# Kernel optimization log

Hardware: AMD Instinct MI355X
Metric: run time of the kernel (lower is better)

The kernel has to match this reference:

```python
import jax, jax.numpy as jnp
import numpy as np

N = 307      # fixed number of graph nodes
C_IN = 5     # input channels
H = 16       # hidden width
K = 6        # Chebyshev orders (K_init=5 -> K+1=6)
LSTM_H = 32  # NL LSTM hidden
B = 512      # batch


def setup_inputs() -> dict:
    key = jax.random.key(0)
    ks = jax.random.split(key, 16)
    s = lambda i, shape, sc=0.1: jax.random.normal(ks[i], shape, jnp.float32) * sc
    return dict(
        flow_x=jax.random.normal(ks[0], (B, N, C_IN), jnp.float32),
        node_emb=jax.random.uniform(ks[1], (N, 10), jnp.float32),  # torch.rand init
        cheb_w=s(2, (K, C_IN, H)),
        cheb_b=jnp.zeros((H,), jnp.float32),
        cou_w=s(3, (C_IN, H)),
        gl_out=s(4, (H, H)),
        gl_fk=s(5, (H, H)),
        gl_tz_w=s(6, (H, H)),
        gl_tz_b=jnp.zeros((H,), jnp.float32),
        lstm_Wih=s(7, (H, 4 * LSTM_H)),
        lstm_b=jnp.zeros((4 * LSTM_H,), jnp.float32),  # b_ih + b_hh combined
        nl_w2=s(8, (LSTM_H, H)),
        c_w=s(9, (H, H)),
        c_b=jnp.zeros((H,), jnp.float32),
        c1_w=s(10, (H, H)),
        c1_b=jnp.zeros((H,), jnp.float32),
    )


def reference(flow_x, node_emb, cheb_w, cheb_b, cou_w, gl_out, gl_fk, gl_tz_w,
              gl_tz_b, lstm_Wih, lstm_b, nl_w2, c_w, c_b, c1_w, c1_b):
    # graph = cosine_similarity(node_embeddings.detach()) -> no grad to node_emb
    E = jax.lax.stop_gradient(node_emb)
    En = E / jnp.linalg.norm(E, axis=1, keepdims=True)
    G = En @ En.T                                            # [N,N]
    # normalized Laplacian L = I - D^-1/2 G D^-1/2
    d = jnp.sum(G, axis=-1) ** -0.5
    I = jnp.eye(N, dtype=G.dtype)
    L = I - (d[:, None] * G) * d[None, :]

    # Chebyshev polynomial stack T_0..T_{K-1}
    Ts = [I, L]
    for _ in range(K - 2):
        Ts.append(2.0 * (L @ Ts[-1]) - Ts[-2])
    polys = jnp.stack(Ts)                                    # [K,N,N]

    out = flow_x @ cou_w                                     # [B,N,H]
    hk = jnp.einsum('knm,bmc->kbnc', polys, flow_x)          # [K,B,N,C]
    output = jnp.einsum('kbnc,kcd->bnd', hk, cheb_w) + cheb_b  # [B,N,H]

    def GL(data):
        o1 = jnp.einsum('nm,bmc->bnc', L, data)
        o3 = jnp.tanh(jnp.tanh(data @ gl_out) @ gl_fk)
        return (o1 - o3) @ gl_tz_w + gl_tz_b

    def NL(data):
        # single-step LSTM cell with zero initial state, then tanh, then linear
        g = data @ lstm_Wih + lstm_b
        i, f, gg, o = jnp.split(g, 4, axis=-1)  # torch gate order i,f,g,o
        c = jax.nn.sigmoid(i) * jnp.tanh(gg)    # c0=0 -> forget term vanishes
        hh = jax.nn.sigmoid(o) * jnp.tanh(c)
        return jnp.tanh(hh) @ nl_w2

    # RK4-like GL diffusion chain: res_1..res_8, step_0, step_1
    prev2, cur = out, output
    for _ in range(10):
        t = GL(cur)
        prev2, cur = cur, cur + 0.5 * t + 0.5 * GL(prev2 + 2.0 * t)
    step_0, step_1 = prev2, cur
    step_00 = step_0 @ c_w + c_b
    step_11 = step_1 @ c1_w + c1_b

    # NL chain: guance_1..guance_10
    t = NL(step_11)
    g = 0.5 * t + step_1 + 0.5 * NL(step_00 + 2.0 * t)
    guances = [g]
    prev2 = step_11
    for _ in range(9):
        t = NL(g)
        new = 0.5 * t + g + 0.5 * NL(prev2 + 2.0 * t)
        prev2, g = g, new
        guances.append(g)

    return jnp.stack(guances, axis=2)  # padding: [B,N,10,H]
```

## Files before the change

kernel.cpp:

```cpp
#include <hip/hip_runtime.h>

#define N 307
#define CIN 5
#define HID 16
#define KORD 6
#define LH 32
#define BATCH 512
#define NP 324
#define NITEM (BATCH * N)

__device__ __forceinline__ float sigmoidf(float x) {
    return __fdividef(1.f, 1.f + __expf(-x));
}
__device__ __forceinline__ float ftanh(float x) {
    float e = __expf(2.f * x);
    return 1.f - __fdividef(2.f, e + 1.f);
}

__global__ __launch_bounds__(320) void k_setup(const float* __restrict__ E,
                                               const float* __restrict__ Wih,
                                               float* __restrict__ Ut,
                                               float* __restrict__ WiT,
                                               float* __restrict__ WgT,
                                               float* __restrict__ WoT) {
    __shared__ float EnS[N * 10];
    __shared__ float sS[10];
    __shared__ float dS[N];
    const int t = threadIdx.x;
    if (t < N) {
        float v[10]; float nrm = 0.f;
        #pragma unroll
        for (int p = 0; p < 10; p++) { v[p] = E[t * 10 + p]; nrm = fmaf(v[p], v[p], nrm); }
        float r = rsqrtf(nrm);
        #pragma unroll
        for (int p = 0; p < 10; p++) EnS[t * 10 + p] = v[p] * r;
    }
    __syncthreads();
    if (t < 10) {
        float s = 0.f;
        for (int nn = 0; nn < N; nn++) s += EnS[nn * 10 + t];
        sS[t] = s;
    }
    __syncthreads();
    if (t < N) {
        float dot = 0.f;
        #pragma unroll
        for (int p = 0; p < 10; p++) dot = fmaf(EnS[t * 10 + p], sS[p], dot);
        dS[t] = rsqrtf(dot);
    }
    __syncthreads();
    for (int i = t; i < 10 * NP; i += 320) {
        int p = i / NP, nn = i - p * NP;
        Ut[i] = (nn < N) ? dS[nn] * EnS[nn * 10 + p] : 0.f;
    }
    for (int i = t; i < LH * HID; i += 320) {
        int j = i >> 4, h = i & 15;
        WiT[i] = Wih[h * 4 * LH + j];
        WgT[i] = Wih[h * 4 * LH + 2 * LH + j];
        WoT[i] = Wih[h * 4 * LH + 3 * LH + j];
    }
}

__device__ __forceinline__ void reduce5(const float* __restrict__ Ub,
                                        const float* __restrict__ Xb,
                                        float* __restrict__ Sp,
                                        float* __restrict__ Sb, int t) {
    const int o = t % 50, sg = t / 50;
    if (sg < 6) {
        const int p = o / 5, c = o - (o / 5) * 5;
        int n0 = sg * 52, n1 = n0 + 52; if (n1 > N) n1 = N;
        const float* up = Ub + p * NP;
        const float* xp = Xb + c * NP;
        float acc = 0.f;
        #pragma unroll 4
        for (int nn = n0; nn < n1; nn++) acc = fmaf(up[nn], xp[nn], acc);
        Sp[t] = acc;
    }
    __syncthreads();
    if (t < 50) {
        float s = 0.f;
        #pragma unroll
        for (int sgi = 0; sgi < 6; sgi++) s += Sp[t + 50 * sgi];
        Sb[t] = s;
    }
    __syncthreads();
}

__device__ __forceinline__ void reduce16(const float* __restrict__ Ub,
                                         const float* __restrict__ Vb,
                                         float* __restrict__ Sp,
                                         float* __restrict__ Sb, int t) {
    const int o = t % 160, sg = t / 160;
    const int p = o >> 4, c = o & 15;
    const float4* up = (const float4*)(Ub + p * NP + sg * 160);
    const float4* xp = (const float4*)(Vb + c * NP + sg * 160);
    float a0 = 0.f, a1 = 0.f;
    #pragma unroll 8
    for (int q = 0; q < 40; q += 2) {
        float4 u0 = up[q], x0 = xp[q];
        a0 = fmaf(u0.x, x0.x, a0); a0 = fmaf(u0.y, x0.y, a0);
        a0 = fmaf(u0.z, x0.z, a0); a0 = fmaf(u0.w, x0.w, a0);
        float4 u1 = up[q + 1], x1 = xp[q + 1];
        a1 = fmaf(u1.x, x1.x, a1); a1 = fmaf(u1.y, x1.y, a1);
        a1 = fmaf(u1.z, x1.z, a1); a1 = fmaf(u1.w, x1.w, a1);
    }
    Sp[t] = a0 + a1;
    __syncthreads();
    if (t < 160) Sb[t] = Sp[t] + Sp[t + 160];
    __syncthreads();
}

__device__ __forceinline__ void glcore(const float* __restrict__ v,
                                       const float* __restrict__ U,
                                       const float* __restrict__ Sb,
                                       const float* __restrict__ wo,
                                       const float* __restrict__ wf,
                                       const float* __restrict__ wt,
                                       const float* __restrict__ bt,
                                       float* __restrict__ z) {
    float o1[HID];
    #pragma unroll
    for (int h = 0; h < HID; h++) o1[h] = v[h];
    #pragma unroll
    for (int p = 0; p < 10; p++) {
        float u = U[p];
        const float4* srow = (const float4*)(Sb + p * HID);
        float4 s0 = srow[0], s1 = srow[1], s2 = srow[2], s3 = srow[3];
        o1[0]  = fmaf(-u, s0.x, o1[0]);  o1[1]  = fmaf(-u, s0.y, o1[1]);
        o1[2]  = fmaf(-u, s0.z, o1[2]);  o1[3]  = fmaf(-u, s0.w, o1[3]);
        o1[4]  = fmaf(-u, s1.x, o1[4]);  o1[5]  = fmaf(-u, s1.y, o1[5]);
        o1[6]  = fmaf(-u, s1.z, o1[6]);  o1[7]  = fmaf(-u, s1.w, o1[7]);
        o1[8]  = fmaf(-u, s2.x, o1[8]);  o1[9]  = fmaf(-u, s2.y, o1[9]);
        o1[10] = fmaf(-u, s2.z, o1[10]); o1[11] = fmaf(-u, s2.w, o1[11]);
        o1[12] = fmaf(-u, s3.x, o1[12]); o1[13] = fmaf(-u, s3.y, o1[13]);
        o1[14] = fmaf(-u, s3.z, o1[14]); o1[15] = fmaf(-u, s3.w, o1[15]);
    }
    float y[HID] = {};
    #pragma unroll
    for (int h2 = 0; h2 < HID; h2++) {
        float xv = v[h2];
        #pragma unroll
        for (int h = 0; h < HID; h++) y[h] = fmaf(xv, wo[h2 * HID + h], y[h]);
    }
    #pragma unroll
    for (int h = 0; h < HID; h++) y[h] = ftanh(y[h]);
    float y2[HID] = {};
    #pragma unroll
    for (int h2 = 0; h2 < HID; h2++) {
        float xv = y[h2];
        #pragma unroll
        for (int h = 0; h < HID; h++) y2[h] = fmaf(xv, wf[h2 * HID + h], y2[h]);
    }
    #pragma unroll
    for (int h = 0; h < HID; h++) z[h] = bt[h];
    #pragma unroll
    for (int h2 = 0; h2 < HID; h2++) {
        float vv = o1[h2] - ftanh(y2[h2]);
        #pragma unroll
        for (int h = 0; h < HID; h++) z[h] = fmaf(vv, wt[h2 * HID + h], z[h]);
    }
}

__global__ __launch_bounds__(320, 3) void k_gl(
    const float* __restrict__ flow, const float* __restrict__ Ut,
    const float* __restrict__ cheb_w, const float* __restrict__ cheb_b,
    const float* __restrict__ cou_w,
    const float* __restrict__ gl_wo, const float* __restrict__ gl_wf,
    const float* __restrict__ gl_wt, const float* __restrict__ gl_bt,
    const float* __restrict__ c_w, const float* __restrict__ c_b,
    const float* __restrict__ c1_w, const float* __restrict__ c1_b,
    float* __restrict__ out) {
    __shared__ __align__(16) float Ub[10 * NP];
    __shared__ __align__(16) float Vb[HID * NP];
    __shared__ __align__(16) float Sp[320];
    __shared__ __align__(16) float Sb[10 * HID];
    const int t = threadIdx.x, b = blockIdx.x;
    const bool act = t < N;

    for (int i = t; i < 10 * NP; i += 320) Ub[i] = Ut[i];
    for (int i = t; i < HID * NP; i += 320) Vb[i] = 0.f;
    __syncthreads();
    for (int i = t; i < N * CIN; i += 320) {
        int nn = i / CIN, c = i - nn * CIN;
        Vb[c * NP + nn] = flow[(size_t)b * N * CIN + i];
    }
    __syncthreads();

    float U[10], prev2[HID], cur[HID], tk0[CIN], tk1[CIN];
    if (act) {
        #pragma unroll
        for (int p = 0; p < 10; p++) U[p] = Ub[p * NP + t];
        float xv[CIN];
        #pragma unroll
        for (int c = 0; c < CIN; c++) { xv[c] = Vb[c * NP + t]; tk0[c] = xv[c]; }
        #pragma unroll
        for (int h = 0; h < HID; h++) {
            float s = 0.f, s2 = cheb_b[h];
            #pragma unroll
            for (int c = 0; c < CIN; c++) {
                s = fmaf(xv[c], cou_w[c * HID + h], s);
                s2 = fmaf(xv[c], cheb_w[c * HID + h], s2);
            }
            prev2[h] = s;
            cur[h] = s2;
        }
    }
    reduce5(Ub, Vb, Sp, Sb, t);
    if (act) {
        #pragma unroll
        for (int c = 0; c < CIN; c++) {
            float s = tk0[c];
            #pragma unroll
            for (int p = 0; p < 10; p++) s = fmaf(-U[p], Sb[p * CIN + c], s);
            tk1[c] = s;
        }
        #pragma unroll
        for (int c = 0; c < CIN; c++) {
            float v = tk1[c];
            #pragma unroll
            for (int h = 0; h < HID; h++)
                cur[h] = fmaf(v, cheb_w[CIN * HID + c * HID + h], cur[h]);
        }
    }
    for (int k = 2; k < KORD; k++) {
        if (act) {
            #pragma unroll
            for (int c = 0; c < CIN; c++) Vb[c * NP + t] = tk1[c];
        }
        __syncthreads();
        reduce5(Ub, Vb, Sp, Sb, t);
        if (act) {
            #pragma unroll
            for (int c = 0; c < CIN; c++) {
                float lt = tk1[c];
                #pragma unroll
                for (int p = 0; p < 10; p++) lt = fmaf(-U[p], Sb[p * CIN + c], lt);
                float tn = 2.f * lt - tk0[c];
                tk0[c] = tk1[c];
                tk1[c] = tn;
            }
            #pragma unroll
            for (int c = 0; c < CIN; c++) {
                float v = tk1[c];
                #pragma unroll
                for (int h = 0; h < HID; h++)
                    cur[h] = fmaf(v, cheb_w[(k * CIN + c) * HID + h], cur[h]);
            }
        }
    }

    for (int it = 0; it < 10; it++) {
        if (act) {
            #pragma unroll
            for (int h = 0; h < HID; h++) Vb[h * NP + t] = cur[h];
        }
        __syncthreads();
        reduce16(Ub, Vb, Sp, Sb, t);
        float tt[HID], wv[HID];
        if (act) {
            glcore(cur, U, Sb, gl_wo, gl_wf, gl_wt, gl_bt, tt);
            #pragma unroll
            for (int h = 0; h < HID; h++) wv[h] = fmaf(2.f, tt[h], prev2[h]);
            #pragma unroll
            for (int h = 0; h < HID; h++) Vb[h * NP + t] = wv[h];
        }
        __syncthreads();
        reduce16(Ub, Vb, Sp, Sb, t);
        if (act) {
            float uu[HID];
            glcore(wv, U, Sb, gl_wo, gl_wf, gl_wt, gl_bt, uu);
            #pragma unroll
            for (int h = 0; h < HID; h++) {
                float nc = cur[h] + 0.5f * (tt[h] + uu[h]);
                prev2[h] = cur[h];
                cur[h] = nc;
            }
        }
    }

    if (act) {
        float s00[HID], s11[HID];
        #pragma unroll
        for (int h = 0; h < HID; h++) { s00[h] = c_b[h]; s11[h] = c1_b[h]; }
        #pragma unroll
        for (int h2 = 0; h2 < HID; h2++) {
            float a = prev2[h2], c2v = cur[h2];
            #pragma unroll
            for (int h = 0; h < HID; h++) {
                s00[h] = fmaf(a, c_w[h2 * HID + h], s00[h]);
                s11[h] = fmaf(c2v, c1_w[h2 * HID + h], s11[h]);
            }
        }
        float* ob = out + (size_t)(b * N + t) * 160;
        float4* wq = (float4*)ob;
        wq[0] = make_float4(s00[0], s00[1], s00[2], s00[3]);
        wq[1] = make_float4(s00[4], s00[5], s00[6], s00[7]);
        wq[2] = make_float4(s00[8], s00[9], s00[10], s00[11]);
        wq[3] = make_float4(s00[12], s00[13], s00[14], s00[15]);
        wq[4] = make_float4(s11[0], s11[1], s11[2], s11[3]);
        wq[5] = make_float4(s11[4], s11[5], s11[6], s11[7]);
        wq[6] = make_float4(s11[8], s11[9], s11[10], s11[11]);
        wq[7] = make_float4(s11[12], s11[13], s11[14], s11[15]);
        wq[8] = make_float4(cur[0], cur[1], cur[2], cur[3]);
        wq[9] = make_float4(cur[4], cur[5], cur[6], cur[7]);
        wq[10] = make_float4(cur[8], cur[9], cur[10], cur[11]);
        wq[11] = make_float4(cur[12], cur[13], cur[14], cur[15]);
    }
}

__device__ __forceinline__ void nl_eval(const float* __restrict__ x,
                                        const float* __restrict__ WiT,
                                        const float* __restrict__ WgT,
                                        const float* __restrict__ WoT,
                                        const float* __restrict__ w2,
                                        const float* __restrict__ bS,
                                        float* __restrict__ outv) {
    #pragma unroll
    for (int h = 0; h < HID; h++) outv[h] = 0.f;
    #pragma unroll 2
    for (int j = 0; j < LH; j++) {
        float gi = bS[j], gg = bS[2 * LH + j], go = bS[3 * LH + j];
        const float4* wi = (const float4*)(WiT + j * HID);
        const float4* wg = (const float4*)(WgT + j * HID);
        const float4* wo4 = (const float4*)(WoT + j * HID);
        #pragma unroll
        for (int q = 0; q < 4; q++) {
            float4 a = wi[q], bb = wg[q], cc = wo4[q];
            gi = fmaf(x[4 * q + 0], a.x, gi); gi = fmaf(x[4 * q + 1], a.y, gi);
            gi = fmaf(x[4 * q + 2], a.z, gi); gi = fmaf(x[4 * q + 3], a.w, gi);
            gg = fmaf(x[4 * q + 0], bb.x, gg); gg = fmaf(x[4 * q + 1], bb.y, gg);
            gg = fmaf(x[4 * q + 2], bb.z, gg); gg = fmaf(x[4 * q + 3], bb.w, gg);
            go = fmaf(x[4 * q + 0], cc.x, go); go = fmaf(x[4 * q + 1], cc.y, go);
            go = fmaf(x[4 * q + 2], cc.z, go); go = fmaf(x[4 * q + 3], cc.w, go);
        }
        float c = sigmoidf(gi) * ftanh(gg);
        float hh = sigmoidf(go) * ftanh(c);
        float th = ftanh(hh);
        const float4* w2r = (const float4*)(w2 + j * HID);
        #pragma unroll
        for (int q = 0; q < 4; q++) {
            float4 a = w2r[q];
            outv[4 * q + 0] = fmaf(th, a.x, outv[4 * q + 0]);
            outv[4 * q + 1] = fmaf(th, a.y, outv[4 * q + 1]);
            outv[4 * q + 2] = fmaf(th, a.z, outv[4 * q + 2]);
            outv[4 * q + 3] = fmaf(th, a.w, outv[4 * q + 3]);
        }
    }
}

__global__ __launch_bounds__(256, 3) void k_nl(
    const float* __restrict__ WiT, const float* __restrict__ WgT,
    const float* __restrict__ WoT, const float* __restrict__ bih,
    const float* __restrict__ w2, float* __restrict__ out) {
    const int item = blockIdx.x * 256 + threadIdx.x;
    if (item >= NITEM) return;
    float* ob = out + (size_t)item * 160;

    float s00[HID], s11[HID], curf[HID];
    {
        const float4* rq = (const float4*)ob;
        float4 a0 = rq[0], a1 = rq[1], a2 = rq[2], a3 = rq[3];
        float4 b0 = rq[4], b1 = rq[5], b2 = rq[6], b3 = rq[7];
        float4 c0 = rq[8], c1 = rq[9], c2 = rq[10], c3 = rq[11];
        s00[0] = a0.x; s00[1] = a0.y; s00[2] = a0.z; s00[3] = a0.w;
        s00[4] = a1.x; s00[5] = a1.y; s00[6] = a1.z; s00[7] = a1.w;
        s00[8] = a2.x; s00[9] = a2.y; s00[10] = a2.z; s00[11] = a2.w;
        s00[12] = a3.x; s00[13] = a3.y; s00[14] = a3.z; s00[15] = a3.w;
        s11[0] = b0.x; s11[1] = b0.y; s11[2] = b0.z; s11[3] = b0.w;
        s11[4] = b1.x; s11[5] = b1.y; s11[6] = b1.z; s11[7] = b1.w;
        s11[8] = b2.x; s11[9] = b2.y; s11[10] = b2.z; s11[11] = b2.w;
        s11[12] = b3.x; s11[13] = b3.y; s11[14] = b3.z; s11[15] = b3.w;
        curf[0] = c0.x; curf[1] = c0.y; curf[2] = c0.z; curf[3] = c0.w;
        curf[4] = c1.x; curf[5] = c1.y; curf[6] = c1.z; curf[7] = c1.w;
        curf[8] = c2.x; curf[9] = c2.y; curf[10] = c2.z; curf[11] = c2.w;
        curf[12] = c3.x; curf[13] = c3.y; curf[14] = c3.z; curf[15] = c3.w;
    }

    float tt[HID], uu[HID], g[HID], p2[HID];
    nl_eval(s11, WiT, WgT, WoT, w2, bih, tt);
    #pragma unroll
    for (int h = 0; h < HID; h++) s00[h] = fmaf(2.f, tt[h], s00[h]);
    nl_eval(s00, WiT, WgT, WoT, w2, bih, uu);
    #pragma unroll
    for (int h = 0; h < HID; h++) {
        g[h] = curf[h] + 0.5f * (tt[h] + uu[h]);
        p2[h] = s11[h];
    }
    {
        float4* wq = (float4*)ob;
        wq[0] = make_float4(g[0], g[1], g[2], g[3]);
        wq[1] = make_float4(g[4], g[5], g[6], g[7]);
        wq[2] = make_float4(g[8], g[9], g[10], g[11]);
        wq[3] = make_float4(g[12], g[13], g[14], g[15]);
    }
    for (int i = 1; i < 10; i++) {
        nl_eval(g, WiT, WgT, WoT, w2, bih, tt);
        #pragma unroll
        for (int h = 0; h < HID; h++) p2[h] = fmaf(2.f, tt[h], p2[h]);
        nl_eval(p2, WiT, WgT, WoT, w2, bih, uu);
        #pragma unroll
        for (int h = 0; h < HID; h++) {
            float ng = g[h] + 0.5f * (tt[h] + uu[h]);
            p2[h] = g[h];
            g[h] = ng;
        }
        float4* wq = (float4*)(ob + i * HID);
        wq[0] = make_float4(g[0], g[1], g[2], g[3]);
        wq[1] = make_float4(g[4], g[5], g[6], g[7]);
        wq[2] = make_float4(g[8], g[9], g[10], g[11]);
        wq[3] = make_float4(g[12], g[13], g[14], g[15]);
    }
}

extern "C" void kernel_launch(void* const* d_in, const int* in_sizes, int n_in,
                              void* d_out, int out_size, void* d_ws, size_t ws_size,
                              hipStream_t stream) {
    const float* flow   = (const float*)d_in[0];
    const float* emb    = (const float*)d_in[1];
    const float* cheb_w = (const float*)d_in[2];
    const float* cheb_b = (const float*)d_in[3];
    const float* cou_w  = (const float*)d_in[4];
    const float* gl_out = (const float*)d_in[5];
    const float* gl_fk  = (const float*)d_in[6];
    const float* gl_tzw = (const float*)d_in[7];
    const float* gl_tzb = (const float*)d_in[8];
    const float* Wih    = (const float*)d_in[9];
    const float* lb     = (const float*)d_in[10];
    const float* w2     = (const float*)d_in[11];
    const float* c_w    = (const float*)d_in[12];
    const float* c_b    = (const float*)d_in[13];
    const float* c1_w   = (const float*)d_in[14];
    const float* c1_b   = (const float*)d_in[15];
    float* out = (float*)d_out;
    float* ws  = (float*)d_ws;

    float* Ut  = ws;
    float* WiT = ws + 3264;
    float* WgT = WiT + 512;
    float* WoT = WgT + 512;

    k_setup<<<1, 320, 0, stream>>>(emb, Wih, Ut, WiT, WgT, WoT);
    k_gl<<<BATCH, 320, 0, stream>>>(flow, Ut, cheb_w, cheb_b, cou_w,
                                    gl_out, gl_fk, gl_tzw, gl_tzb,
                                    c_w, c_b, c1_w, c1_b, out);
    k_nl<<<NITEM / 256, 256, 0, stream>>>(WiT, WgT, WoT, lb, w2, out);
}
```

Measured before the change: 951.0 us.

## Split NL LSTM hidden units across two threads per item with shared-memory reduction

The NL kernel now assigns two threads to each (batch, node) item, each computing half of the 32 LSTM hidden units. The partial output vectors are summed through a shared-memory buffer, fenced by two block barriers per NL evaluation. This doubles the thread count and halves the serial per-thread work, aiming to raise occupancy and latency hiding in a kernel that previously launched only about 614 blocks. In exchange it adds 40 barrier-guarded shared-memory exchanges per thread, and both halves redundantly hold and update the full state vectors.

```diff
diff --git a/kernel.cpp b/kernel.cpp
--- a/kernel.cpp
+++ b/kernel.cpp
@@ -8,6 +8,8 @@
 #define BATCH 512
 #define NP 324
 #define NITEM (BATCH * N)
+#define NLB 1228
+#define XS 17
 
 __device__ __forceinline__ float sigmoidf(float x) {
     return __fdividef(1.f, 1.f + __expf(-x));
@@ -308,18 +310,22 @@
     }
 }
 
-__device__ __forceinline__ void nl_eval(const float* __restrict__ x,
-                                        const float* __restrict__ WiT,
-                                        const float* __restrict__ WgT,
-                                        const float* __restrict__ WoT,
-                                        const float* __restrict__ w2,
-                                        const float* __restrict__ bS,
-                                        float* __restrict__ outv) {
-    #pragma unroll
-    for (int h = 0; h < HID; h++) outv[h] = 0.f;
+__device__ __forceinline__ void nl_eval_h(const float* __restrict__ x, int j0,
+                                          const float* __restrict__ WiT,
+                                          const float* __restrict__ WgT,
+                                          const float* __restrict__ WoT,
+                                          const float* __restrict__ w2,
+                                          const float* __restrict__ bih,
+                                          float* __restrict__ Xs,
+                                          int slot, int half,
+                                          float* __restrict__ outv) {
+    float part[HID];
+    #pragma unroll
+    for (int h = 0; h < HID; h++) part[h] = 0.f;
     #pragma unroll 2
-    for (int j = 0; j < LH; j++) {
-        float gi = bS[j], gg = bS[2 * LH + j], go = bS[3 * LH + j];
+    for (int jj = 0; jj < 16; jj++) {
+        const int j = j0 + jj;
+        float gi = bih[j], gg = bih[2 * LH + j], go = bih[3 * LH + j];
         const float4* wi = (const float4*)(WiT + j * HID);
         const float4* wg = (const float4*)(WgT + j * HID);
         const float4* wo4 = (const float4*)(WoT + j * HID);
@@ -340,20 +346,33 @@
         #pragma unroll
         for (int q = 0; q < 4; q++) {
             float4 a = w2r[q];
-            outv[4 * q + 0] = fmaf(th, a.x, outv[4 * q + 0]);
-            outv[4 * q + 1] = fmaf(th, a.y, outv[4 * q + 1]);
-            outv[4 * q + 2] = fmaf(th, a.z, outv[4 * q + 2]);
-            outv[4 * q + 3] = fmaf(th, a.w, outv[4 * q + 3]);
-        }
-    }
+            part[4 * q + 0] = fmaf(th, a.x, part[4 * q + 0]);
+            part[4 * q + 1] = fmaf(th, a.y, part[4 * q + 1]);
+            part[4 * q + 2] = fmaf(th, a.z, part[4 * q + 2]);
+            part[4 * q + 3] = fmaf(th, a.w, part[4 * q + 3]);
+        }
+    }
+    float* my = Xs + half * (128 * XS) + slot * XS;
+    #pragma unroll
+    for (int h = 0; h < HID; h++) my[h] = part[h];
+    __syncthreads();
+    const float* r0 = Xs + slot * XS;
+    const float* r1 = Xs + 128 * XS + slot * XS;
+    #pragma unroll
+    for (int h = 0; h < HID; h++) outv[h] = r0[h] + r1[h];
+    __syncthreads();
 }
 
 __global__ __launch_bounds__(256, 3) void k_nl(
     const float* __restrict__ WiT, const float* __restrict__ WgT,
     const float* __restrict__ WoT, const float* __restrict__ bih,
     const float* __restrict__ w2, float* __restrict__ out) {
-    const int item = blockIdx.x * 256 + threadIdx.x;
-    if (item >= NITEM) return;
+    __shared__ float Xs[2 * 128 * XS];
+    const int t = threadIdx.x;
+    const int half = t >> 7;
+    const int slot = t & 127;
+    const int item = blockIdx.x * 128 + slot;
+    const int j0 = half * 16;
     float* ob = out + (size_t)item * 160;
 
     float s00[HID], s11[HID], curf[HID];
@@ -377,16 +396,16 @@
     }
 
     float tt[HID], uu[HID], g[HID], p2[HID];
-    nl_eval(s11, WiT, WgT, WoT, w2, bih, tt);
+    nl_eval_h(s11, j0, WiT, WgT, WoT, w2, bih, Xs, slot, half, tt);
     #pragma unroll
     for (int h = 0; h < HID; h++) s00[h] = fmaf(2.f, tt[h], s00[h]);
-    nl_eval(s00, WiT, WgT, WoT, w2, bih, uu);
+    nl_eval_h(s00, j0, WiT, WgT, WoT, w2, bih, Xs, slot, half, uu);
     #pragma unroll
     for (int h = 0; h < HID; h++) {
         g[h] = curf[h] + 0.5f * (tt[h] + uu[h]);
         p2[h] = s11[h];
     }
-    {
+    if (half == 0) {
         float4* wq = (float4*)ob;
         wq[0] = make_float4(g[0], g[1], g[2], g[3]);
         wq[1] = make_float4(g[4], g[5], g[6], g[7]);
@@ -394,21 +413,23 @@
         wq[3] = make_float4(g[12], g[13], g[14], g[15]);
     }
     for (int i = 1; i < 10; i++) {
-        nl_eval(g, WiT, WgT, WoT, w2, bih, tt);
+        nl_eval_h(g, j0, WiT, WgT, WoT, w2, bih, Xs, slot, half, tt);
         #pragma unroll
         for (int h = 0; h < HID; h++) p2[h] = fmaf(2.f, tt[h], p2[h]);
-        nl_eval(p2, WiT, WgT, WoT, w2, bih, uu);
+        nl_eval_h(p2, j0, WiT, WgT, WoT, w2, bih, Xs, slot, half, uu);
         #pragma unroll
         for (int h = 0; h < HID; h++) {
             float ng = g[h] + 0.5f * (tt[h] + uu[h]);
             p2[h] = g[h];
             g[h] = ng;
         }
-        float4* wq = (float4*)(ob + i * HID);
-        wq[0] = make_float4(g[0], g[1], g[2], g[3]);
-        wq[1] = make_float4(g[4], g[5], g[6], g[7]);
-        wq[2] = make_float4(g[8], g[9], g[10], g[11]);
-        wq[3] = make_float4(g[12], g[13], g[14], g[15]);
+        if (half == 0) {
+            float4* wq = (float4*)(ob + i * HID);
+            wq[0] = make_float4(g[0], g[1], g[2], g[3]);
+            wq[1] = make_float4(g[4], g[5], g[6], g[7]);
+            wq[2] = make_float4(g[8], g[9], g[10], g[11]);
+            wq[3] = make_float4(g[12], g[13], g[14], g[15]);
+        }
     }
 }
 
@@ -443,5 +464,5 @@
     k_gl<<<BATCH, 320, 0, stream>>>(flow, Ut, cheb_w, cheb_b, cou_w,
                                     gl_out, gl_fk, gl_tzw, gl_tzb,
                                     c_w, c_b, c1_w, c1_b, out);
-    k_nl<<<NITEM / 256, 256, 0, stream>>>(WiT, WgT, WoT, lb, w2, out);
-}
+    k_nl<<<NLB, 256, 0, stream>>>(WiT, WgT, WoT, lb, w2, out);
+}
```

After: 1.254 ms. +31.9%, slower.
